# Optimization experiments

Measured on AMD Instinct MI355X. Metric: run time of the kernel, lower is better.

The kernel has to match this reference:

```python
import jax, jax.numpy as jnp
import numpy as np

# thresholds from options['dist_threshold'] (init-time constants)
THRESHOLDS = jnp.array([0.5, 1.0], dtype=jnp.float32)

B, N, D, K = 16, 16384, 64, 64  # batch, h*w pixels, embed dim, n templates
N_CLASSES = 21


def setup_inputs() -> dict:
    key = jax.random.key(0)
    k1, k2, k3 = jax.random.split(key, 3)
    frame_embeddings = jax.random.normal(k1, (B, N, D), dtype=jnp.float32)
    templates = jax.random.normal(k2, (K, N, D), dtype=jnp.float32)
    template_classes = jax.random.randint(k3, (K,), 0, N_CLASSES, dtype=jnp.int64)
    return {
        "frame_embeddings": frame_embeddings,
        "templates": templates,
        "template_classes": template_classes,
    }


def reference(frame_embeddings, templates, template_classes):
    # Squared euclidean distance per pixel to each template, vectorized over K
    # [B,K,N,D] broadcast intermediate the torch loop also never materializes).
    x2 = jnp.sum(frame_embeddings * frame_embeddings, axis=-1)      # [B, N]
    t2 = jnp.sum(templates * templates, axis=-1)                    # [K, N]
    xt = jnp.einsum('bnd,knd->bkn', frame_embeddings, templates)    # [B, K, N]
    dists = x2[:, None, :] + t2[None, :, :] - 2.0 * xt              # [B, K, N]

    min_dists = jnp.min(dists, axis=1)                              # [B, N]
    min_idx = jnp.argmin(dists, axis=1)                             # [B, N]

    # One boolean mask per threshold, stacked: [T, B, N]
    masks = min_dists[None, :, :] <= THRESHOLDS[:, None, None]
    pred_classes = template_classes[min_idx]                        # [B, N]
    return masks, min_dists, pred_classes
```

## Files before the change

kernel.cpp:

```cpp
#include <hip/hip_runtime.h>
#include <stdint.h>


#define BB 16
#define NN 16384
#define DD 64
#define KK 64

typedef float v2f __attribute__((ext_vector_type(2)));

template <int PAT>
__device__ __forceinline__ float swz(float v) {
    return __int_as_float(__builtin_amdgcn_ds_swizzle(__float_as_int(v), PAT));
}

__global__ __launch_bounds__(256, 1)
void openset_kernel(const float* __restrict__ x,
                    const float* __restrict__ tmpl,
                    const int*   __restrict__ tcls,
                    float*       __restrict__ out) {
    const int lane = threadIdx.x & 63;
    const int wv   = threadIdx.x >> 6;
    const int n    = ((blockIdx.x & 7) << 11) | (blockIdx.x >> 3);
    const int d8   = lane & 7;
    const int k8   = lane >> 3;
    const int wb   = wv * 4;

    v2f xlo[4][2], xhi[4][2];
#pragma unroll
    for (int i = 0; i < 4; ++i)
#pragma unroll
        for (int h = 0; h < 2; ++h) {
            float4 xv = *(const float4*)(x + ((size_t)(wb + i) * NN + n) * DD
                                           + 4 * d8 + 32 * h);
            xlo[i][h] = (v2f){xv.x, xv.y};
            xhi[i][h] = (v2f){xv.z, xv.w};
        }

    const float* tb = tmpl + (size_t)k8 * NN * DD + (size_t)n * DD + 4 * d8;

    float bestd  = 3.4e38f;
    int   bestcb = 0;

    const bool u0 = (lane & 1) != 0;
    const bool u1 = (lane & 2) != 0;

#pragma unroll
    for (int cb = 0; cb < KK; cb += 8) {
        float4 t0 = *(const float4*)(tb + (size_t)cb * NN * DD);
        float4 t1 = *(const float4*)(tb + (size_t)cb * NN * DD + 32);
        v2f tl0 = (v2f){t0.x, t0.y}, th0 = (v2f){t0.z, t0.w};
        v2f tl1 = (v2f){t1.x, t1.y}, th1 = (v2f){t1.z, t1.w};

        float p[4];
#pragma unroll
        for (int i = 0; i < 4; ++i) {
            v2f dl0 = xlo[i][0] - tl0, dh0 = xhi[i][0] - th0;
            v2f dl1 = xlo[i][1] - tl1, dh1 = xhi[i][1] - th1;
            v2f s0v = dl0 * dl0 + dh0 * dh0;
            v2f s1v = dl1 * dl1 + dh1 * dh1;
            v2f sv  = s0v + s1v;
            p[i] = sv.x + sv.y;
        }

        float a0 = u0 ? p[2] : p[0];
        float s0 = u0 ? p[0] : p[2];
        float a1 = u0 ? p[3] : p[1];
        float s1 = u0 ? p[1] : p[3];
        float q0 = a0 + swz<0x041F>(s0);
        float q1 = a1 + swz<0x041F>(s1);
        float a  = u1 ? q1 : q0;
        float s  = u1 ? q0 : q1;
        float r  = a + swz<0x081F>(s);
        r += swz<0x101F>(r);

        if (r < bestd) { bestd = r; bestcb = cb; }
    }

    int bestk = bestcb + k8;

#pragma unroll
    for (int m = 8; m < 64; m <<= 1) {
        float od = __shfl_xor(bestd, m);
        int   ok = __shfl_xor(bestk, m);
        if (od < bestd || (od == bestd && ok < bestk)) { bestd = od; bestk = ok; }
    }

    if (lane < 4) {
        const int b = wb + 2 * (lane & 1) + ((lane >> 1) & 1);
        const size_t BN = (size_t)BB * NN;
        const size_t o  = (size_t)b * NN + n;
        out[o]          = (bestd <= 0.5f) ? 1.0f : 0.0f;
        out[BN + o]     = (bestd <= 1.0f) ? 1.0f : 0.0f;
        out[2 * BN + o] = bestd;
        out[3 * BN + o] = (float)tcls[bestk];
    }
}

extern "C" void kernel_launch(void* const* d_in, const int* in_sizes, int n_in,
                              void* d_out, int out_size, void* d_ws, size_t ws_size,
                              hipStream_t stream) {
    const float* x    = (const float*)d_in[0];
    const float* tmpl = (const float*)d_in[1];
    const int*   tcls = (const int*)d_in[2];
    float* out = (float*)d_out;

    dim3 grid(NN);
    dim3 block(256);
    openset_kernel<<<grid, block, 0, stream>>>(x, tmpl, tcls, out);
}
```

Baseline: 420.1 us.

## Map one template per lane and one pixel per wave, reduce min across lanes

Work is remapped so each wave owns one pixel and each lane owns one template. The lane loads its template row into registers and loops over all 16 batch frames, accumulating squared distances. This replaces the ds_swizzle partial-sum reductions with a per-batch wave-wide min and a ballot-based argmin. Launch bounds are raised to two blocks per CU and the grid shrinks to a quarter. The x loads become uniform broadcasts across the wave, and the template loads become strided per lane rather than coalesced, which changes the memory access pattern.

```diff
diff --git a/kernel.cpp b/kernel.cpp
--- a/kernel.cpp
+++ b/kernel.cpp
@@ -9,87 +9,65 @@
 
 typedef float v2f __attribute__((ext_vector_type(2)));
 
-template <int PAT>
-__device__ __forceinline__ float swz(float v) {
-    return __int_as_float(__builtin_amdgcn_ds_swizzle(__float_as_int(v), PAT));
-}
-
-__global__ __launch_bounds__(256, 1)
+__global__ __launch_bounds__(256, 2)
 void openset_kernel(const float* __restrict__ x,
                     const float* __restrict__ tmpl,
                     const int*   __restrict__ tcls,
                     float*       __restrict__ out) {
     const int lane = threadIdx.x & 63;
     const int wv   = threadIdx.x >> 6;
-    const int n    = ((blockIdx.x & 7) << 11) | (blockIdx.x >> 3);
-    const int d8   = lane & 7;
-    const int k8   = lane >> 3;
-    const int wb   = wv * 4;
+    const int p = (int)(((blockIdx.x & 7) << 11) | ((blockIdx.x >> 3) << 2)) | wv;
 
-    v2f xlo[4][2], xhi[4][2];
+    const float* tb = tmpl + ((size_t)lane << 20) + (size_t)p * DD;
+    const float* xb = x + (size_t)p * DD;
+
+    v2f acc[BB];
 #pragma unroll
-    for (int i = 0; i < 4; ++i)
-#pragma unroll
-        for (int h = 0; h < 2; ++h) {
-            float4 xv = *(const float4*)(x + ((size_t)(wb + i) * NN + n) * DD
-                                           + 4 * d8 + 32 * h);
-            xlo[i][h] = (v2f){xv.x, xv.y};
-            xhi[i][h] = (v2f){xv.z, xv.w};
-        }
-
-    const float* tb = tmpl + (size_t)k8 * NN * DD + (size_t)n * DD + 4 * d8;
-
-    float bestd  = 3.4e38f;
-    int   bestcb = 0;
-
-    const bool u0 = (lane & 1) != 0;
-    const bool u1 = (lane & 2) != 0;
+    for (int b = 0; b < BB; ++b) acc[b] = (v2f){0.f, 0.f};
 
 #pragma unroll
-    for (int cb = 0; cb < KK; cb += 8) {
-        float4 t0 = *(const float4*)(tb + (size_t)cb * NN * DD);
-        float4 t1 = *(const float4*)(tb + (size_t)cb * NN * DD + 32);
-        v2f tl0 = (v2f){t0.x, t0.y}, th0 = (v2f){t0.z, t0.w};
-        v2f tl1 = (v2f){t1.x, t1.y}, th1 = (v2f){t1.z, t1.w};
-
-        float p[4];
+    for (int h = 0; h < 2; ++h) {
+        v2f t[16];
 #pragma unroll
-        for (int i = 0; i < 4; ++i) {
-            v2f dl0 = xlo[i][0] - tl0, dh0 = xhi[i][0] - th0;
-            v2f dl1 = xlo[i][1] - tl1, dh1 = xhi[i][1] - th1;
-            v2f s0v = dl0 * dl0 + dh0 * dh0;
-            v2f s1v = dl1 * dl1 + dh1 * dh1;
-            v2f sv  = s0v + s1v;
-            p[i] = sv.x + sv.y;
+        for (int j = 0; j < 8; ++j) {
+            float4 tv = *(const float4*)(tb + 32 * h + 4 * j);
+            t[2 * j]     = (v2f){tv.x, tv.y};
+            t[2 * j + 1] = (v2f){tv.z, tv.w};
         }
-
-        float a0 = u0 ? p[2] : p[0];
-        float s0 = u0 ? p[0] : p[2];
-        float a1 = u0 ? p[3] : p[1];
-        float s1 = u0 ? p[1] : p[3];
-        float q0 = a0 + swz<0x041F>(s0);
-        float q1 = a1 + swz<0x041F>(s1);
-        float a  = u1 ? q1 : q0;
-        float s  = u1 ? q0 : q1;
-        float r  = a + swz<0x081F>(s);
-        r += swz<0x101F>(r);
-
-        if (r < bestd) { bestd = r; bestcb = cb; }
+#pragma unroll
+        for (int b = 0; b < BB; ++b) {
+            const float* xr = xb + ((size_t)b << 20) + 32 * h;
+            v2f a0 = (v2f){0.f, 0.f};
+            v2f a1 = (v2f){0.f, 0.f};
+#pragma unroll
+            for (int j = 0; j < 8; ++j) {
+                float4 xv = *(const float4*)(xr + 4 * j);
+                v2f d0 = (v2f){xv.x, xv.y} - t[2 * j];
+                v2f d1 = (v2f){xv.z, xv.w} - t[2 * j + 1];
+                a0 += d0 * d0;
+                a1 += d1 * d1;
+            }
+            acc[b] += a0 + a1;
+        }
     }
 
-    int bestk = bestcb + k8;
-
+    float bestd = 0.f;
+    int   bestk = 0;
 #pragma unroll
-    for (int m = 8; m < 64; m <<= 1) {
-        float od = __shfl_xor(bestd, m);
-        int   ok = __shfl_xor(bestk, m);
-        if (od < bestd || (od == bestd && ok < bestk)) { bestd = od; bestk = ok; }
+    for (int b = 0; b < BB; ++b) {
+        const float dme = acc[b].x + acc[b].y;
+        float m = dme;
+#pragma unroll
+        for (int i = 1; i < 64; i <<= 1)
+            m = fminf(m, __shfl_xor(m, i));
+        const unsigned long long tie = __ballot(dme == m);
+        const int ks = __ffsll(tie) - 1;
+        if (lane == b) { bestd = m; bestk = ks; }
     }
 
-    if (lane < 4) {
-        const int b = wb + 2 * (lane & 1) + ((lane >> 1) & 1);
+    if (lane < BB) {
         const size_t BN = (size_t)BB * NN;
-        const size_t o  = (size_t)b * NN + n;
+        const size_t o  = (size_t)lane * NN + p;
         out[o]          = (bestd <= 0.5f) ? 1.0f : 0.0f;
         out[BN + o]     = (bestd <= 1.0f) ? 1.0f : 0.0f;
         out[2 * BN + o] = bestd;
@@ -105,7 +83,7 @@
     const int*   tcls = (const int*)d_in[2];
     float* out = (float*)d_out;
 
-    dim3 grid(NN);
+    dim3 grid(NN / 4);
     dim3 block(256);
     openset_kernel<<<grid, block, 0, stream>>>(x, tmpl, tcls, out);
 }
```

New measurement: 598.7 us. 42.5% more time.
